# Performance work log

Measured on AMD Instinct MI355X. Metric: run time of the kernel, lower is better.

## Reference

```python
import jax, jax.numpy as jnp
import numpy as np
from jax import lax
import math

D_MODEL, D_STATE, D_CONV, D_INNER, DT_RANK = 1024, 16, 4, 2048, 64
BATCH, SEQLEN = 2, 2048


def setup_inputs() -> dict:
    key = jax.random.key(0)
    ks = jax.random.split(key, 10)
    s = 0.02
    x = jax.random.normal(ks[0], (BATCH, SEQLEN, D_MODEL), jnp.float32)
    W_in = jax.random.normal(ks[1], (D_MODEL, 2 * D_INNER), jnp.float32) * s
    conv_w = jax.random.normal(ks[2], (D_INNER, 1, D_CONV), jnp.float32) * 0.2
    conv_b = jnp.zeros((D_INNER,), jnp.float32)
    W_x = jax.random.normal(ks[3], (D_INNER, DT_RANK + 2 * D_STATE), jnp.float32) * s
    W_dt = jax.random.normal(ks[4], (DT_RANK, D_INNER), jnp.float32) * s
    # dt bias init as in the torch module: inverse-softplus of dt ~ logU(1e-3, 1e-1)
    u = jax.random.uniform(ks[5], (D_INNER,), jnp.float32)
    dt = jnp.clip(jnp.exp(u * (math.log(0.1) - math.log(0.001)) + math.log(0.001)), 1e-4)
    b_dt = dt + jnp.log(-jnp.expm1(-dt))
    A_log = jnp.log(jnp.tile(jnp.arange(1, D_STATE + 1, dtype=jnp.float32)[None, :], (D_INNER, 1)))
    D = jnp.ones((D_INNER,), jnp.float32)
    W_out = jax.random.normal(ks[6], (D_INNER, D_MODEL), jnp.float32) * s
    return {"x": x, "W_in": W_in, "conv_w": conv_w, "conv_b": conv_b, "W_x": W_x,
            "W_dt": W_dt, "b_dt": b_dt, "A_log": A_log, "D": D, "W_out": W_out}


def _forward(x, W_in, conv_w, conv_b, W_x, W_dt, b_dt, A_log, D, W_out):
    b, l, _ = x.shape
    d_inner, d_state = A_log.shape
    d_conv = conv_w.shape[-1]
    dt_rank = W_dt.shape[0]

    xz = x @ W_in                                  # (b, l, 2*d_inner)
    xi, z = jnp.split(xz, 2, axis=-1)

    # depthwise causal conv1d (torch pads both sides by d_conv-1 then slices [:l])
    xc = jnp.transpose(xi, (0, 2, 1))              # (b, d_inner, l)
    xc = lax.conv_general_dilated(
        xc, conv_w, window_strides=(1,), padding=[(d_conv - 1, 0)],
        feature_group_count=d_inner,
        dimension_numbers=("NCH", "OIH", "NCH"))
    xc = xc + conv_b[None, :, None]
    xi = jax.nn.silu(jnp.transpose(xc, (0, 2, 1)))  # (b, l, d_inner)

    x_dbl = xi @ W_x                                # (b, l, dt_rank + 2*d_state)
    dt, B, C = jnp.split(x_dbl, [dt_rank, dt_rank + d_state], axis=-1)
    dt = jax.nn.softplus(dt @ W_dt + b_dt)          # (b, l, d_inner)
    A = -jnp.exp(A_log)                             # (d_inner, d_state)

    def step(h, inp):
        dt_t, B_t, C_t, x_t = inp                   # (b,d),(b,n),(b,n),(b,d)
        dA = jnp.exp(dt_t[..., None] * A)           # (b, d, n)
        dB = dt_t[..., None] * B_t[:, None, :]      # (b, d, n)
        h = dA * h + dB * x_t[..., None]
        y = jnp.einsum("bdn,bn->bd", h, C_t) + D * x_t
        return h, y

    xs = (jnp.transpose(dt, (1, 0, 2)), jnp.transpose(B, (1, 0, 2)),
          jnp.transpose(C, (1, 0, 2)), jnp.transpose(xi, (1, 0, 2)))
    h0 = jnp.zeros((b, d_inner, d_state), x.dtype)
    _, ys = lax.scan(step, h0, xs)                  # ys: (l, b, d_inner)
    y = jnp.transpose(ys, (1, 0, 2))

    y = y * jax.nn.silu(z)
    return y @ W_out                                # (b, l, d_model)


def reference(x, W_in, conv_w, conv_b, W_x, W_dt, b_dt, A_log, D, W_out):
    return _forward(x, W_in, conv_w, conv_b, W_x, W_dt, b_dt, A_log, D, W_out)
```

## Files before the change

### kernel.cpp

```cpp
#include <hip/hip_runtime.h>
#include <math.h>


#define D_INNER 2048
#define D_STATE 16
#define SEQLEN  2048
#define NBATCH  2
#define NCHUNK  32
#define CHUNKLEN (SEQLEN / NCHUNK)

using f32x4 = __attribute__((ext_vector_type(4))) float;
using s16x8 = __attribute__((ext_vector_type(8))) short;

__device__ __forceinline__ float siluf(float x) {
  return x / (1.f + __expf(-x));
}
__device__ __forceinline__ float softplusf(float x) {
  return fmaxf(x, 0.f) + log1pf(__expf(-fabsf(x)));
}

__device__ __forceinline__ void split_pair(float f0, float f1,
                                           unsigned& hw, unsigned& lw) {
  unsigned b0 = __float_as_uint(f0), b1 = __float_as_uint(f1);
  hw = (b0 >> 16) | (b1 & 0xFFFF0000u);
  float r0 = f0 - __uint_as_float(b0 & 0xFFFF0000u);
  float r1 = f1 - __uint_as_float(b1 & 0xFFFF0000u);
  unsigned c0 = __float_as_uint(r0); c0 += 0x7FFFu + ((c0 >> 16) & 1u);
  unsigned c1 = __float_as_uint(r1); c1 += 0x7FFFu + ((c1 >> 16) & 1u);
  lw = (c0 >> 16) | (c1 & 0xFFFF0000u);
}

__global__ __launch_bounds__(256) void packsplit_k(
    const float* __restrict__ in, unsigned* __restrict__ out)
{
  size_t g = (size_t)blockIdx.x * 256 + threadIdx.x;
  float f[32];
#pragma unroll
  for (int q = 0; q < 8; ++q)
    *(float4*)&f[q * 4] = *(const float4*)(in + g * 32 + q * 4);
  unsigned* o = out + g * 32;
#pragma unroll
  for (int j = 0; j < 16; ++j) {
    unsigned hw, lw;
    split_pair(f[2 * j], f[2 * j + 1], hw, lw);
    o[j] = hw; o[16 + j] = lw;
  }
}

__global__ __launch_bounds__(256) void transpack_k(
    const float* __restrict__ in, unsigned* __restrict__ out, int K, int N)
{
  __shared__ float tile[32][257];
  const int tid = threadIdx.x;
  const int nb = blockIdx.x * 256;
  const int kc = blockIdx.y;
#pragma unroll 8
  for (int ky = 0; ky < 32; ++ky)
    tile[ky][tid] = in[(size_t)(kc * 32 + ky) * N + nb + tid];
  __syncthreads();
  unsigned* o = out + ((size_t)(nb + tid) * (K >> 5) + kc) * 32;
#pragma unroll
  for (int j = 0; j < 16; ++j) {
    unsigned hw, lw;
    split_pair(tile[2 * j][tid], tile[2 * j + 1][tid], hw, lw);
    o[j] = hw; o[16 + j] = lw;
  }
}

__global__ __launch_bounds__(128) void transpack_wx_k(
    const float* __restrict__ Wx, unsigned* __restrict__ out)
{
  const int n = threadIdx.x;
  const int kc = blockIdx.x;
  float f[32];
#pragma unroll
  for (int j = 0; j < 32; ++j)
    f[j] = (n < 96) ? Wx[(size_t)(kc * 32 + j) * 96 + n] : 0.f;
  unsigned* o = out + ((size_t)n * 64 + kc) * 32;
#pragma unroll
  for (int j = 0; j < 16; ++j) {
    unsigned hw, lw;
    split_pair(f[2 * j], f[2 * j + 1], hw, lw);
    o[j] = hw; o[16 + j] = lw;
  }
}

__global__ __launch_bounds__(256, 2) void mgemm_split(
    const unsigned short* __restrict__ A, const unsigned short* __restrict__ Bt,
    float* __restrict__ C, int M, int N, int K, int ldc)
{
  __shared__ s16x8 AsV[128 * 8];
  __shared__ s16x8 BsV[128 * 8];

  const int tid = threadIdx.x;
  const int wv  = tid >> 6;
  const int ln  = tid & 63;
  const int wr  = wv >> 1, wc = wv & 1;
  const int m0  = blockIdx.y * 128, n0 = blockIdx.x * 128;
  const int K32 = K >> 5;

  const int rr = ln & 15;
  const int ko = ln >> 4;
  const int sh = ko ^ (rr & 7);
  const int sl = (4 | ko) ^ (rr & 7);

  const int srow  = ln >> 3;
  const int sslot = (ln & 7) ^ srow;

  f32x4 acc[4][4];
#pragma unroll
  for (int i = 0; i < 4; i++)
#pragma unroll
    for (int j = 0; j < 4; j++) acc[i][j] = (f32x4)0.f;

  for (int ktc = 0; ktc < K32; ++ktc) {
    __syncthreads();
#pragma unroll
    for (int t = 0; t < 4; ++t) {
      int i = wv * 4 + t;
      const unsigned short* ga =
          A + ((size_t)(m0 + i * 8 + srow) * K32 + ktc) * 64 + sslot * 8;
      const unsigned short* gb =
          Bt + ((size_t)(n0 + i * 8 + srow) * K32 + ktc) * 64 + sslot * 8;
      __builtin_amdgcn_global_load_lds(
          (const __attribute__((address_space(1))) void*)ga,
          (__attribute__((address_space(3))) void*)((char*)AsV + i * 1024), 16, 0, 0);
      __builtin_amdgcn_global_load_lds(
          (const __attribute__((address_space(1))) void*)gb,
          (__attribute__((address_space(3))) void*)((char*)BsV + i * 1024), 16, 0, 0);
    }
    __syncthreads();

    s16x8 ah[4], al[4], bh[4], bl[4];
#pragma unroll
    for (int mi = 0; mi < 4; ++mi) {
      int r = wr * 64 + mi * 16 + rr;
      ah[mi] = AsV[r * 8 + sh];
      al[mi] = AsV[r * 8 + sl];
    }
#pragma unroll
    for (int ni = 0; ni < 4; ++ni) {
      int c = wc * 64 + ni * 16 + rr;
      bh[ni] = BsV[c * 8 + sh];
      bl[ni] = BsV[c * 8 + sl];
    }
#pragma unroll
    for (int mi = 0; mi < 4; ++mi)
#pragma unroll
      for (int ni = 0; ni < 4; ++ni) {
        acc[mi][ni] = __builtin_amdgcn_mfma_f32_16x16x32_bf16(ah[mi], bh[ni], acc[mi][ni], 0, 0, 0);
        acc[mi][ni] = __builtin_amdgcn_mfma_f32_16x16x32_bf16(ah[mi], bl[ni], acc[mi][ni], 0, 0, 0);
        acc[mi][ni] = __builtin_amdgcn_mfma_f32_16x16x32_bf16(al[mi], bh[ni], acc[mi][ni], 0, 0, 0);
      }
  }

  const int orow = (ln >> 4) * 4;
#pragma unroll
  for (int mi = 0; mi < 4; ++mi)
#pragma unroll
    for (int ni = 0; ni < 4; ++ni) {
      int rowg = m0 + wr * 64 + mi * 16 + orow;
      int colg = n0 + wc * 64 + ni * 16 + rr;
#pragma unroll
      for (int i = 0; i < 4; ++i)
        C[(size_t)(rowg + i) * ldc + colg] = acc[mi][ni][i];
    }
}

__global__ __launch_bounds__(256, 2) void xdbl_mfma_k(
    const unsigned short* __restrict__ A, const unsigned short* __restrict__ Bt,
    float* __restrict__ P)
{
  __shared__ s16x8 AsV[128 * 8];
  __shared__ s16x8 BsV[128 * 8];

  const int tid = threadIdx.x;
  const int wv  = tid >> 6;
  const int ln  = tid & 63;
  const int wr  = wv >> 1, wc = wv & 1;
  const int kz  = blockIdx.x;
  const int m0  = blockIdx.y * 128;
  const int K32 = 64;

  const int rr = ln & 15;
  const int ko = ln >> 4;
  const int sh = ko ^ (rr & 7);
  const int sl = (4 | ko) ^ (rr & 7);
  const int srow  = ln >> 3;
  const int sslot = (ln & 7) ^ srow;

  f32x4 acc[4][4];
#pragma unroll
  for (int i = 0; i < 4; i++)
#pragma unroll
    for (int j = 0; j < 4; j++) acc[i][j] = (f32x4)0.f;

  for (int ktc = kz * 8; ktc < kz * 8 + 8; ++ktc) {
    __syncthreads();
#pragma unroll
    for (int t = 0; t < 4; ++t) {
      int i = wv * 4 + t;
      const unsigned short* ga =
          A + ((size_t)(m0 + i * 8 + srow) * K32 + ktc) * 64 + sslot * 8;
      const unsigned short* gb =
          Bt + ((size_t)(i * 8 + srow) * K32 + ktc) * 64 + sslot * 8;
      __builtin_amdgcn_global_load_lds(
          (const __attribute__((address_space(1))) void*)ga,
          (__attribute__((address_space(3))) void*)((char*)AsV + i * 1024), 16, 0, 0);
      __builtin_amdgcn_global_load_lds(
          (const __attribute__((address_space(1))) void*)gb,
          (__attribute__((address_space(3))) void*)((char*)BsV + i * 1024), 16, 0, 0);
    }
    __syncthreads();

    s16x8 ah[4], al[4], bh[4], bl[4];
#pragma unroll
    for (int mi = 0; mi < 4; ++mi) {
      int r = wr * 64 + mi * 16 + rr;
      ah[mi] = AsV[r * 8 + sh];
      al[mi] = AsV[r * 8 + sl];
    }
#pragma unroll
    for (int ni = 0; ni < 4; ++ni) {
      int c = wc * 64 + ni * 16 + rr;
      bh[ni] = BsV[c * 8 + sh];
      bl[ni] = BsV[c * 8 + sl];
    }
#pragma unroll
    for (int mi = 0; mi < 4; ++mi)
#pragma unroll
      for (int ni = 0; ni < 4; ++ni) {
        acc[mi][ni] = __builtin_amdgcn_mfma_f32_16x16x32_bf16(ah[mi], bh[ni], acc[mi][ni], 0, 0, 0);
        acc[mi][ni] = __builtin_amdgcn_mfma_f32_16x16x32_bf16(ah[mi], bl[ni], acc[mi][ni], 0, 0, 0);
        acc[mi][ni] = __builtin_amdgcn_mfma_f32_16x16x32_bf16(al[mi], bh[ni], acc[mi][ni], 0, 0, 0);
      }
  }

  const int orow = (ln >> 4) * 4;
#pragma unroll
  for (int mi = 0; mi < 4; ++mi)
#pragma unroll
    for (int ni = 0; ni < 4; ++ni) {
      int rowg = m0 + wr * 64 + mi * 16 + orow;
      int colg = wc * 64 + ni * 16 + rr;
      if (colg < 96) {
#pragma unroll
        for (int i = 0; i < 4; ++i)
          P[((size_t)kz * 4096 + rowg + i) * 96 + colg] = acc[mi][ni][i];
      }
    }
}

__global__ __launch_bounds__(256) void xdbl_reduce_k(
    const float* __restrict__ P, float* __restrict__ xdbl)
{
  int i = blockIdx.x * 256 + threadIdx.x;
  float s = 0.f;
#pragma unroll
  for (int kz = 0; kz < 8; ++kz) s += P[(size_t)kz * 393216 + i];
  xdbl[i] = s;
}

template <int EPI>
__global__ __launch_bounds__(256, 2) void sgemm_k(
    const float* __restrict__ A, const float* __restrict__ B,
    const float* __restrict__ bias, float* __restrict__ C,
    int M, int N, int K, int lda, int ldb, int ldc)
{
  __shared__ float As[16][132];
  __shared__ float Bs[16][128];

  const int tid = threadIdx.x;
  const int m0 = blockIdx.y * 128;
  const int n0 = blockIdx.x * 128;
  const int tx = tid & 15;
  const int ty = tid >> 4;

  float acc[2][2][4][4];
#pragma unroll
  for (int a = 0; a < 2; a++)
#pragma unroll
    for (int b2 = 0; b2 < 2; b2++)
#pragma unroll
      for (int i = 0; i < 4; i++)
#pragma unroll
        for (int j = 0; j < 4; j++) acc[a][b2][i][j] = 0.f;

  for (int k0 = 0; k0 < K; k0 += 16) {
#pragma unroll
    for (int t = 0; t < 2; ++t) {
      int i = tid + t * 256;
      int row = i >> 2;
      int kq = (i & 3) * 4;
      float4 v = *(const float4*)(A + (size_t)(m0 + row) * lda + k0 + kq);
      As[kq + 0][row] = v.x; As[kq + 1][row] = v.y;
      As[kq + 2][row] = v.z; As[kq + 3][row] = v.w;
    }
#pragma unroll
    for (int t = 0; t < 2; ++t) {
      int i = tid + t * 256;
      int kr = i >> 5;
      int cq = (i & 31) * 4;
      *(float4*)&Bs[kr][cq] = *(const float4*)(B + (size_t)(k0 + kr) * ldb + n0 + cq);
    }
    __syncthreads();
#pragma unroll
    for (int kk = 0; kk < 16; ++kk) {
      float4 a0 = *(const float4*)&As[kk][ty * 4];
      float4 a1 = *(const float4*)&As[kk][64 + ty * 4];
      float4 b0 = *(const float4*)&Bs[kk][tx * 4];
      float4 b1 = *(const float4*)&Bs[kk][64 + tx * 4];
      float av[2][4] = {{a0.x, a0.y, a0.z, a0.w}, {a1.x, a1.y, a1.z, a1.w}};
      float bv[2][4] = {{b0.x, b0.y, b0.z, b0.w}, {b1.x, b1.y, b1.z, b1.w}};
#pragma unroll
      for (int a = 0; a < 2; a++)
#pragma unroll
        for (int i = 0; i < 4; i++)
#pragma unroll
          for (int b2 = 0; b2 < 2; b2++)
#pragma unroll
            for (int j = 0; j < 4; j++)
              acc[a][b2][i][j] = fmaf(av[a][i], bv[b2][j], acc[a][b2][i][j]);
    }
    __syncthreads();
  }

#pragma unroll
  for (int a = 0; a < 2; a++) {
#pragma unroll
    for (int i = 0; i < 4; i++) {
      int row = m0 + a * 64 + ty * 4 + i;
#pragma unroll
      for (int b2 = 0; b2 < 2; b2++) {
        int col = n0 + b2 * 64 + tx * 4;
        float4 v = make_float4(acc[a][b2][i][0], acc[a][b2][i][1],
                               acc[a][b2][i][2], acc[a][b2][i][3]);
        if (EPI == 1) {
          v.x = softplusf(v.x + bias[col + 0]);
          v.y = softplusf(v.y + bias[col + 1]);
          v.z = softplusf(v.z + bias[col + 2]);
          v.w = softplusf(v.w + bias[col + 3]);
        }
        *(float4*)(C + (size_t)row * ldc + col) = v;
      }
    }
  }
}

__global__ __launch_bounds__(256) void conv_silu_k(
    const float* __restrict__ xz, const float* __restrict__ cw,
    const float* __restrict__ cb, float* __restrict__ xi)
{
  int idx = blockIdx.x * 256 + threadIdx.x;
  int d = idx & (D_INNER - 1);
  int row = idx >> 11;
  int l = row & (SEQLEN - 1);
  float4 w = *(const float4*)(cw + d * 4);
  const float wv[4] = {w.x, w.y, w.z, w.w};
  float acc = cb[d];
#pragma unroll
  for (int j = 0; j < 4; j++) {
    int ll = l - 3 + j;
    if (ll >= 0)
      acc = fmaf(wv[j], xz[(size_t)(row - 3 + j) * 4096 + d], acc);
  }
  xi[idx] = siluf(acc);
}

__global__ __launch_bounds__(256) void aprep_k(const float* __restrict__ A_log,
                                               float* __restrict__ A2)
{
  int i = blockIdx.x * 256 + threadIdx.x;
  A2[i] = -__expf(A_log[i]);
}

__global__ __launch_bounds__(256) void scan_pass1(
    const float* __restrict__ dt, const float* __restrict__ xi,
    const float* __restrict__ xdbl, const float* __restrict__ A2,
    float* __restrict__ cP, float* __restrict__ cH)
{
  int d = blockIdx.x * 256 + threadIdx.x;
  int c = blockIdx.y;
  int b = blockIdx.z;
  float a2[D_STATE], h[D_STATE], P[D_STATE];
#pragma unroll
  for (int n = 0; n < D_STATE; n++) {
    a2[n] = A2[d * D_STATE + n];
    h[n] = 0.f;
    P[n] = 1.f;
  }
  int rowbase = b * SEQLEN + c * CHUNKLEN;
  for (int l = 0; l < CHUNKLEN; l++) {
    int row = rowbase + l;
    float dtv = dt[(size_t)row * D_INNER + d];
    float xv = xi[(size_t)row * D_INNER + d];
    float dtx = dtv * xv;
    const float* Bp = xdbl + (size_t)row * 96 + 64;
#pragma unroll
    for (int n = 0; n < D_STATE; n++) {
      float dA = __expf(dtv * a2[n]);
      P[n] *= dA;
      h[n] = fmaf(dA, h[n], dtx * Bp[n]);
    }
  }
  size_t base = ((size_t)(b * D_INNER + d) * NCHUNK + c) * D_STATE;
#pragma unroll
  for (int n = 0; n < D_STATE; n++) {
    cP[base + n] = P[n];
    cH[base + n] = h[n];
  }
}

__global__ __launch_bounds__(256) void scan_pass2(
    const float* __restrict__ cP, float* __restrict__ cH)
{
  int t = blockIdx.x * 256 + threadIdx.x;
  size_t base = (size_t)(t >> 4) * (NCHUNK * D_STATE) + (t & 15);
  float h = 0.f;
  for (int c = 0; c < NCHUNK; c++) {
    size_t idx = base + (size_t)c * D_STATE;
    float Pv = cP[idx];
    float q = cH[idx];
    cH[idx] = h;
    h = fmaf(Pv, h, q);
  }
}

__global__ __launch_bounds__(256) void scan_pass3(
    float* __restrict__ dtyg, const float* __restrict__ xi,
    const float* __restrict__ xdbl, const float* __restrict__ A2,
    const float* __restrict__ cH, const float* __restrict__ Dvec,
    const float* __restrict__ xz)
{
  int d = blockIdx.x * 256 + threadIdx.x;
  int c = blockIdx.y;
  int b = blockIdx.z;
  float a2[D_STATE], h[D_STATE];
  size_t base = ((size_t)(b * D_INNER + d) * NCHUNK + c) * D_STATE;
#pragma unroll
  for (int n = 0; n < D_STATE; n++) {
    a2[n] = A2[d * D_STATE + n];
    h[n] = cH[base + n];
  }
  float Dd = Dvec[d];
  int rowbase = b * SEQLEN + c * CHUNKLEN;
  for (int l = 0; l < CHUNKLEN; l++) {
    int row = rowbase + l;
    float dtv = dtyg[(size_t)row * D_INNER + d];
    float xv = xi[(size_t)row * D_INNER + d];
    float dtx = dtv * xv;
    const float* Bp = xdbl + (size_t)row * 96 + 64;
    const float* Cp = Bp + D_STATE;
    float y = Dd * xv;
#pragma unroll
    for (int n = 0; n < D_STATE; n++) {
      float dA = __expf(dtv * a2[n]);
      h[n] = fmaf(dA, h[n], dtx * Bp[n]);
      y = fmaf(h[n], Cp[n], y);
    }
    float z = xz[(size_t)row * 4096 + D_INNER + d];
    dtyg[(size_t)row * D_INNER + d] = y * siluf(z);
  }
}

extern "C" void kernel_launch(void* const* d_in, const int* in_sizes, int n_in,
                              void* d_out, int out_size, void* d_ws,
                              size_t ws_size, hipStream_t stream)
{
  const float* x     = (const float*)d_in[0];
  const float* W_in  = (const float*)d_in[1];
  const float* cw    = (const float*)d_in[2];
  const float* cb    = (const float*)d_in[3];
  const float* W_x   = (const float*)d_in[4];
  const float* W_dt  = (const float*)d_in[5];
  const float* b_dt  = (const float*)d_in[6];
  const float* A_log = (const float*)d_in[7];
  const float* Dv    = (const float*)d_in[8];
  const float* W_out = (const float*)d_in[9];
  float* out = (float*)d_out;

  float* ws    = (float*)d_ws;
  float* xz    = ws;
  float* xi    = xz + 16777216;
  float* xdbl  = xi + 8388608;
  float* dtyg  = xdbl + 393216;
  float* A2    = dtyg + 8388608;
  float* cP    = A2 + 32768;
  float* cH    = cP + 2097152;

  unsigned* WinTP  = (unsigned*)dtyg;
  unsigned* xP     = (unsigned*)(dtyg + 4194304);
  unsigned* xiP    = (unsigned*)dtyg;
  unsigned* WxTP   = (unsigned*)xdbl;
  float*    Ppart  = cP;
  unsigned* ygP    = (unsigned*)xi;
  unsigned* WoutTP = (unsigned*)cP;

  aprep_k<<<128, 256, 0, stream>>>(A_log, A2);

  transpack_k<<<dim3(16, 32), 256, 0, stream>>>(W_in, WinTP, 1024, 4096);
  packsplit_k<<<512, 256, 0, stream>>>(x, xP);

  mgemm_split<<<dim3(32, 32), 256, 0, stream>>>(
      (const unsigned short*)xP, (const unsigned short*)WinTP, xz,
      4096, 4096, 1024, 4096);

  conv_silu_k<<<32768, 256, 0, stream>>>(xz, cw, cb, xi);

  packsplit_k<<<1024, 256, 0, stream>>>(xi, xiP);
  transpack_wx_k<<<64, 128, 0, stream>>>(W_x, WxTP);
  xdbl_mfma_k<<<dim3(8, 32), 256, 0, stream>>>(
      (const unsigned short*)xiP, (const unsigned short*)WxTP, Ppart);
  xdbl_reduce_k<<<1536, 256, 0, stream>>>(Ppart, xdbl);

  sgemm_k<1><<<dim3(16, 32), 256, 0, stream>>>(xdbl, W_dt, b_dt, dtyg,
                                               4096, 2048, 64, 96, 2048, 2048);

  scan_pass1<<<dim3(8, NCHUNK, NBATCH), 256, 0, stream>>>(dtyg, xi, xdbl, A2, cP, cH);
  scan_pass2<<<256, 256, 0, stream>>>(cP, cH);
  scan_pass3<<<dim3(8, NCHUNK, NBATCH), 256, 0, stream>>>(dtyg, xi, xdbl, A2, cH, Dv, xz);

  packsplit_k<<<1024, 256, 0, stream>>>(dtyg, ygP);
  transpack_k<<<dim3(4, 64), 256, 0, stream>>>(W_out, WoutTP, 2048, 1024);

  mgemm_split<<<dim3(8, 32), 256, 0, stream>>>(
      (const unsigned short*)ygP, (const unsigned short*)WoutTP, out,
      4096, 1024, 2048, 1024);
}
```

Before: 478.8 us.

## Double-buffer LDS in split-bf16 MFMA GEMMs and fuse conv+SiLU with packing

Both split-bf16 MFMA GEMM kernels now use two LDS buffers and prefetch the next K-slice with global_load_lds while computing on the current one. This replaces the two barriers per iteration with a single wait and barrier at the end of each step. Separately, the depthwise conv+SiLU kernel is fused with the bf16 hi/lo packing of xi, removing one full read of xi and one kernel launch. Doubling LDS per block may lower occupancy, and the wait still drains all loads each iteration, so overlap is limited.

```diff
diff --git a/kernel.cpp b/kernel.cpp
--- a/kernel.cpp
+++ b/kernel.cpp
@@ -89,8 +89,8 @@
     const unsigned short* __restrict__ A, const unsigned short* __restrict__ Bt,
     float* __restrict__ C, int M, int N, int K, int ldc)
 {
-  __shared__ s16x8 AsV[128 * 8];
-  __shared__ s16x8 BsV[128 * 8];
+  __shared__ s16x8 AsV[2][128 * 8];
+  __shared__ s16x8 BsV[2][128 * 8];
 
   const int tid = threadIdx.x;
   const int wv  = tid >> 6;
@@ -103,18 +103,10 @@
   const int ko = ln >> 4;
   const int sh = ko ^ (rr & 7);
   const int sl = (4 | ko) ^ (rr & 7);
-
   const int srow  = ln >> 3;
   const int sslot = (ln & 7) ^ srow;
 
-  f32x4 acc[4][4];
-#pragma unroll
-  for (int i = 0; i < 4; i++)
-#pragma unroll
-    for (int j = 0; j < 4; j++) acc[i][j] = (f32x4)0.f;
-
-  for (int ktc = 0; ktc < K32; ++ktc) {
-    __syncthreads();
+  auto stage = [&](int buf, int ktc) {
 #pragma unroll
     for (int t = 0; t < 4; ++t) {
       int i = wv * 4 + t;
@@ -124,25 +116,39 @@
           Bt + ((size_t)(n0 + i * 8 + srow) * K32 + ktc) * 64 + sslot * 8;
       __builtin_amdgcn_global_load_lds(
           (const __attribute__((address_space(1))) void*)ga,
-          (__attribute__((address_space(3))) void*)((char*)AsV + i * 1024), 16, 0, 0);
+          (__attribute__((address_space(3))) void*)((char*)&AsV[buf][0] + i * 1024), 16, 0, 0);
       __builtin_amdgcn_global_load_lds(
           (const __attribute__((address_space(1))) void*)gb,
-          (__attribute__((address_space(3))) void*)((char*)BsV + i * 1024), 16, 0, 0);
-    }
-    __syncthreads();
+          (__attribute__((address_space(3))) void*)((char*)&BsV[buf][0] + i * 1024), 16, 0, 0);
+    }
+  };
+
+  f32x4 acc[4][4];
+#pragma unroll
+  for (int i = 0; i < 4; i++)
+#pragma unroll
+    for (int j = 0; j < 4; j++) acc[i][j] = (f32x4)0.f;
+
+  stage(0, 0);
+  asm volatile("s_waitcnt vmcnt(0)" ::: "memory");
+  __builtin_amdgcn_s_barrier();
+
+  int cur = 0;
+  for (int ktc = 0; ktc < K32; ++ktc) {
+    if (ktc + 1 < K32) stage(cur ^ 1, ktc + 1);
 
     s16x8 ah[4], al[4], bh[4], bl[4];
 #pragma unroll
     for (int mi = 0; mi < 4; ++mi) {
       int r = wr * 64 + mi * 16 + rr;
-      ah[mi] = AsV[r * 8 + sh];
-      al[mi] = AsV[r * 8 + sl];
+      ah[mi] = AsV[cur][r * 8 + sh];
+      al[mi] = AsV[cur][r * 8 + sl];
     }
 #pragma unroll
     for (int ni = 0; ni < 4; ++ni) {
       int c = wc * 64 + ni * 16 + rr;
-      bh[ni] = BsV[c * 8 + sh];
-      bl[ni] = BsV[c * 8 + sl];
+      bh[ni] = BsV[cur][c * 8 + sh];
+      bl[ni] = BsV[cur][c * 8 + sl];
     }
 #pragma unroll
     for (int mi = 0; mi < 4; ++mi)
@@ -152,6 +158,10 @@
         acc[mi][ni] = __builtin_amdgcn_mfma_f32_16x16x32_bf16(ah[mi], bl[ni], acc[mi][ni], 0, 0, 0);
         acc[mi][ni] = __builtin_amdgcn_mfma_f32_16x16x32_bf16(al[mi], bh[ni], acc[mi][ni], 0, 0, 0);
       }
+
+    asm volatile("s_waitcnt lgkmcnt(0) vmcnt(0)" ::: "memory");
+    __builtin_amdgcn_s_barrier();
+    cur ^= 1;
   }
 
   const int orow = (ln >> 4) * 4;
@@ -171,8 +181,8 @@
     const unsigned short* __restrict__ A, const unsigned short* __restrict__ Bt,
     float* __restrict__ P)
 {
-  __shared__ s16x8 AsV[128 * 8];
-  __shared__ s16x8 BsV[128 * 8];
+  __shared__ s16x8 AsV[2][128 * 8];
+  __shared__ s16x8 BsV[2][128 * 8];
 
   const int tid = threadIdx.x;
   const int wv  = tid >> 6;
@@ -189,14 +199,7 @@
   const int srow  = ln >> 3;
   const int sslot = (ln & 7) ^ srow;
 
-  f32x4 acc[4][4];
-#pragma unroll
-  for (int i = 0; i < 4; i++)
-#pragma unroll
-    for (int j = 0; j < 4; j++) acc[i][j] = (f32x4)0.f;
-
-  for (int ktc = kz * 8; ktc < kz * 8 + 8; ++ktc) {
-    __syncthreads();
+  auto stage = [&](int buf, int ktc) {
 #pragma unroll
     for (int t = 0; t < 4; ++t) {
       int i = wv * 4 + t;
@@ -206,25 +209,40 @@
           Bt + ((size_t)(i * 8 + srow) * K32 + ktc) * 64 + sslot * 8;
       __builtin_amdgcn_global_load_lds(
           (const __attribute__((address_space(1))) void*)ga,
-          (__attribute__((address_space(3))) void*)((char*)AsV + i * 1024), 16, 0, 0);
+          (__attribute__((address_space(3))) void*)((char*)&AsV[buf][0] + i * 1024), 16, 0, 0);
       __builtin_amdgcn_global_load_lds(
           (const __attribute__((address_space(1))) void*)gb,
-          (__attribute__((address_space(3))) void*)((char*)BsV + i * 1024), 16, 0, 0);
-    }
-    __syncthreads();
+          (__attribute__((address_space(3))) void*)((char*)&BsV[buf][0] + i * 1024), 16, 0, 0);
+    }
+  };
+
+  f32x4 acc[4][4];
+#pragma unroll
+  for (int i = 0; i < 4; i++)
+#pragma unroll
+    for (int j = 0; j < 4; j++) acc[i][j] = (f32x4)0.f;
+
+  const int kbeg = kz * 8, kend = kz * 8 + 8;
+  stage(0, kbeg);
+  asm volatile("s_waitcnt vmcnt(0)" ::: "memory");
+  __builtin_amdgcn_s_barrier();
+
+  int cur = 0;
+  for (int ktc = kbeg; ktc < kend; ++ktc) {
+    if (ktc + 1 < kend) stage(cur ^ 1, ktc + 1);
 
     s16x8 ah[4], al[4], bh[4], bl[4];
 #pragma unroll
     for (int mi = 0; mi < 4; ++mi) {
       int r = wr * 64 + mi * 16 + rr;
-      ah[mi] = AsV[r * 8 + sh];
-      al[mi] = AsV[r * 8 + sl];
+      ah[mi] = AsV[cur][r * 8 + sh];
+      al[mi] = AsV[cur][r * 8 + sl];
     }
 #pragma unroll
     for (int ni = 0; ni < 4; ++ni) {
       int c = wc * 64 + ni * 16 + rr;
-      bh[ni] = BsV[c * 8 + sh];
-      bl[ni] = BsV[c * 8 + sl];
+      bh[ni] = BsV[cur][c * 8 + sh];
+      bl[ni] = BsV[cur][c * 8 + sl];
     }
 #pragma unroll
     for (int mi = 0; mi < 4; ++mi)
@@ -234,6 +252,10 @@
         acc[mi][ni] = __builtin_amdgcn_mfma_f32_16x16x32_bf16(ah[mi], bl[ni], acc[mi][ni], 0, 0, 0);
         acc[mi][ni] = __builtin_amdgcn_mfma_f32_16x16x32_bf16(al[mi], bh[ni], acc[mi][ni], 0, 0, 0);
       }
+
+    asm volatile("s_waitcnt lgkmcnt(0) vmcnt(0)" ::: "memory");
+    __builtin_amdgcn_s_barrier();
+    cur ^= 1;
   }
 
   const int orow = (ln >> 4) * 4;
@@ -347,24 +369,58 @@
   }
 }
 
-__global__ __launch_bounds__(256) void conv_silu_k(
+__global__ __launch_bounds__(256) void conv_silu_pack_k(
     const float* __restrict__ xz, const float* __restrict__ cw,
-    const float* __restrict__ cb, float* __restrict__ xi)
-{
-  int idx = blockIdx.x * 256 + threadIdx.x;
-  int d = idx & (D_INNER - 1);
-  int row = idx >> 11;
+    const float* __restrict__ cb, float* __restrict__ xi,
+    unsigned* __restrict__ xiP)
+{
+  int g = blockIdx.x * 256 + threadIdx.x;
+  int ck = g & 63;
+  int row = g >> 6;
   int l = row & (SEQLEN - 1);
-  float4 w = *(const float4*)(cw + d * 4);
-  const float wv[4] = {w.x, w.y, w.z, w.w};
-  float acc = cb[d];
-#pragma unroll
-  for (int j = 0; j < 4; j++) {
-    int ll = l - 3 + j;
-    if (ll >= 0)
-      acc = fmaf(wv[j], xz[(size_t)(row - 3 + j) * 4096 + d], acc);
-  }
-  xi[idx] = siluf(acc);
+  int d0 = ck * 32;
+
+  float* xo = xi + (size_t)row * D_INNER + d0;
+  unsigned* po = xiP + (size_t)g * 32;
+
+#pragma unroll
+  for (int q = 0; q < 4; ++q) {
+    int dq = d0 + q * 8;
+    float acc[8];
+    float4 wv4[8];
+#pragma unroll
+    for (int e = 0; e < 8; ++e) {
+      wv4[e] = *(const float4*)(cw + (size_t)(dq + e) * 4);
+      acc[e] = cb[dq + e];
+    }
+#pragma unroll
+    for (int j = 0; j < 4; ++j) {
+      int ll = l - 3 + j;
+      if (ll >= 0) {
+        const float* src = xz + (size_t)(row - 3 + j) * 4096 + dq;
+        float4 v0 = *(const float4*)(src);
+        float4 v1 = *(const float4*)(src + 4);
+        float in[8] = {v0.x, v0.y, v0.z, v0.w, v1.x, v1.y, v1.z, v1.w};
+#pragma unroll
+        for (int e = 0; e < 8; ++e) {
+          float w = (j == 0) ? wv4[e].x : (j == 1) ? wv4[e].y
+                   : (j == 2) ? wv4[e].z : wv4[e].w;
+          acc[e] = fmaf(w, in[e], acc[e]);
+        }
+      }
+    }
+#pragma unroll
+    for (int e = 0; e < 8; ++e) acc[e] = siluf(acc[e]);
+    *(float4*)(xo + q * 8)     = make_float4(acc[0], acc[1], acc[2], acc[3]);
+    *(float4*)(xo + q * 8 + 4) = make_float4(acc[4], acc[5], acc[6], acc[7]);
+#pragma unroll
+    for (int p = 0; p < 4; ++p) {
+      unsigned hw, lw;
+      split_pair(acc[2 * p], acc[2 * p + 1], hw, lw);
+      po[q * 4 + p] = hw;
+      po[16 + q * 4 + p] = lw;
+    }
+  }
 }
 
 __global__ __launch_bounds__(256) void aprep_k(const float* __restrict__ A_log,
@@ -505,9 +561,8 @@
       (const unsigned short*)xP, (const unsigned short*)WinTP, xz,
       4096, 4096, 1024, 4096);
 
-  conv_silu_k<<<32768, 256, 0, stream>>>(xz, cw, cb, xi);
-
-  packsplit_k<<<1024, 256, 0, stream>>>(xi, xiP);
+  conv_silu_pack_k<<<1024, 256, 0, stream>>>(xz, cw, cb, xi, xiP);
+
   transpack_wx_k<<<64, 128, 0, stream>>>(W_x, WxTP);
   xdbl_mfma_k<<<dim3(8, 32), 256, 0, stream>>>(
       (const unsigned short*)xiP, (const unsigned short*)WxTP, Ppart);
```

New measurement: 535.6 us. +11.9%, slower.

## Double-buffer LDS tiles in split-bf16 GEMM kernels to overlap loads with MFMA

Applied to the files above, without the earlier changes.

Both the main split-bf16 GEMM and the x_dbl GEMM now keep two LDS buffers and prefetch the k-tile two steps ahead with global_load_lds. Partial vmcnt waits plus raw s_barrier replace the two __syncthreads per iteration. The aim is to hide global-memory latency behind the MFMA work. In exchange LDS use per block doubles, which may limit occupancy. Correctness also depends on the hand-chosen vmcnt count and on the ordering of LDS reads relative to the barriers.

```diff
diff --git a/kernel.cpp b/kernel.cpp
--- a/kernel.cpp
+++ b/kernel.cpp
@@ -89,8 +89,8 @@
     const unsigned short* __restrict__ A, const unsigned short* __restrict__ Bt,
     float* __restrict__ C, int M, int N, int K, int ldc)
 {
-  __shared__ s16x8 AsV[128 * 8];
-  __shared__ s16x8 BsV[128 * 8];
+  __shared__ s16x8 AsV[2][128 * 8];
+  __shared__ s16x8 BsV[2][128 * 8];
 
   const int tid = threadIdx.x;
   const int wv  = tid >> 6;
@@ -103,18 +103,10 @@
   const int ko = ln >> 4;
   const int sh = ko ^ (rr & 7);
   const int sl = (4 | ko) ^ (rr & 7);
-
   const int srow  = ln >> 3;
   const int sslot = (ln & 7) ^ srow;
 
-  f32x4 acc[4][4];
-#pragma unroll
-  for (int i = 0; i < 4; i++)
-#pragma unroll
-    for (int j = 0; j < 4; j++) acc[i][j] = (f32x4)0.f;
-
-  for (int ktc = 0; ktc < K32; ++ktc) {
-    __syncthreads();
+  auto stage = [&](int buf, int ktc) {
 #pragma unroll
     for (int t = 0; t < 4; ++t) {
       int i = wv * 4 + t;
@@ -124,25 +116,42 @@
           Bt + ((size_t)(n0 + i * 8 + srow) * K32 + ktc) * 64 + sslot * 8;
       __builtin_amdgcn_global_load_lds(
           (const __attribute__((address_space(1))) void*)ga,
-          (__attribute__((address_space(3))) void*)((char*)AsV + i * 1024), 16, 0, 0);
+          (__attribute__((address_space(3))) void*)((char*)&AsV[buf][0] + i * 1024), 16, 0, 0);
       __builtin_amdgcn_global_load_lds(
           (const __attribute__((address_space(1))) void*)gb,
-          (__attribute__((address_space(3))) void*)((char*)BsV + i * 1024), 16, 0, 0);
-    }
-    __syncthreads();
+          (__attribute__((address_space(3))) void*)((char*)&BsV[buf][0] + i * 1024), 16, 0, 0);
+    }
+  };
+
+  f32x4 acc[4][4];
+#pragma unroll
+  for (int i = 0; i < 4; i++)
+#pragma unroll
+    for (int j = 0; j < 4; j++) acc[i][j] = (f32x4)0.f;
+
+  stage(0, 0);
+  stage(1, 1);
+
+  int cur = 0;
+  for (int ktc = 0; ktc < K32; ++ktc) {
+    if (ktc + 1 < K32)
+      asm volatile("s_waitcnt vmcnt(8)" ::: "memory");
+    else
+      asm volatile("s_waitcnt vmcnt(0)" ::: "memory");
+    __builtin_amdgcn_s_barrier();
 
     s16x8 ah[4], al[4], bh[4], bl[4];
 #pragma unroll
     for (int mi = 0; mi < 4; ++mi) {
       int r = wr * 64 + mi * 16 + rr;
-      ah[mi] = AsV[r * 8 + sh];
-      al[mi] = AsV[r * 8 + sl];
+      ah[mi] = AsV[cur][r * 8 + sh];
+      al[mi] = AsV[cur][r * 8 + sl];
     }
 #pragma unroll
     for (int ni = 0; ni < 4; ++ni) {
       int c = wc * 64 + ni * 16 + rr;
-      bh[ni] = BsV[c * 8 + sh];
-      bl[ni] = BsV[c * 8 + sl];
+      bh[ni] = BsV[cur][c * 8 + sh];
+      bl[ni] = BsV[cur][c * 8 + sl];
     }
 #pragma unroll
     for (int mi = 0; mi < 4; ++mi)
@@ -152,6 +161,10 @@
         acc[mi][ni] = __builtin_amdgcn_mfma_f32_16x16x32_bf16(ah[mi], bl[ni], acc[mi][ni], 0, 0, 0);
         acc[mi][ni] = __builtin_amdgcn_mfma_f32_16x16x32_bf16(al[mi], bh[ni], acc[mi][ni], 0, 0, 0);
       }
+
+    __builtin_amdgcn_s_barrier();
+    if (ktc + 2 < K32) stage(cur, ktc + 2);
+    cur ^= 1;
   }
 
   const int orow = (ln >> 4) * 4;
@@ -171,8 +184,8 @@
     const unsigned short* __restrict__ A, const unsigned short* __restrict__ Bt,
     float* __restrict__ P)
 {
-  __shared__ s16x8 AsV[128 * 8];
-  __shared__ s16x8 BsV[128 * 8];
+  __shared__ s16x8 AsV[2][128 * 8];
+  __shared__ s16x8 BsV[2][128 * 8];
 
   const int tid = threadIdx.x;
   const int wv  = tid >> 6;
@@ -189,14 +202,7 @@
   const int srow  = ln >> 3;
   const int sslot = (ln & 7) ^ srow;
 
-  f32x4 acc[4][4];
-#pragma unroll
-  for (int i = 0; i < 4; i++)
-#pragma unroll
-    for (int j = 0; j < 4; j++) acc[i][j] = (f32x4)0.f;
-
-  for (int ktc = kz * 8; ktc < kz * 8 + 8; ++ktc) {
-    __syncthreads();
+  auto stage = [&](int buf, int ktc) {
 #pragma unroll
     for (int t = 0; t < 4; ++t) {
       int i = wv * 4 + t;
@@ -206,25 +212,43 @@
           Bt + ((size_t)(i * 8 + srow) * K32 + ktc) * 64 + sslot * 8;
       __builtin_amdgcn_global_load_lds(
           (const __attribute__((address_space(1))) void*)ga,
-          (__attribute__((address_space(3))) void*)((char*)AsV + i * 1024), 16, 0, 0);
+          (__attribute__((address_space(3))) void*)((char*)&AsV[buf][0] + i * 1024), 16, 0, 0);
       __builtin_amdgcn_global_load_lds(
           (const __attribute__((address_space(1))) void*)gb,
-          (__attribute__((address_space(3))) void*)((char*)BsV + i * 1024), 16, 0, 0);
-    }
-    __syncthreads();
+          (__attribute__((address_space(3))) void*)((char*)&BsV[buf][0] + i * 1024), 16, 0, 0);
+    }
+  };
+
+  f32x4 acc[4][4];
+#pragma unroll
+  for (int i = 0; i < 4; i++)
+#pragma unroll
+    for (int j = 0; j < 4; j++) acc[i][j] = (f32x4)0.f;
+
+  const int kbeg = kz * 8, kend = kz * 8 + 8;
+  stage(0, kbeg);
+  stage(1, kbeg + 1);
+
+  int cur = 0;
+  for (int ktc = kbeg; ktc < kend; ++ktc) {
+    if (ktc + 1 < kend)
+      asm volatile("s_waitcnt vmcnt(8)" ::: "memory");
+    else
+      asm volatile("s_waitcnt vmcnt(0)" ::: "memory");
+    __builtin_amdgcn_s_barrier();
 
     s16x8 ah[4], al[4], bh[4], bl[4];
 #pragma unroll
     for (int mi = 0; mi < 4; ++mi) {
       int r = wr * 64 + mi * 16 + rr;
-      ah[mi] = AsV[r * 8 + sh];
-      al[mi] = AsV[r * 8 + sl];
+      ah[mi] = AsV[cur][r * 8 + sh];
+      al[mi] = AsV[cur][r * 8 + sl];
     }
 #pragma unroll
     for (int ni = 0; ni < 4; ++ni) {
       int c = wc * 64 + ni * 16 + rr;
-      bh[ni] = BsV[c * 8 + sh];
-      bl[ni] = BsV[c * 8 + sl];
+      bh[ni] = BsV[cur][c * 8 + sh];
+      bl[ni] = BsV[cur][c * 8 + sl];
     }
 #pragma unroll
     for (int mi = 0; mi < 4; ++mi)
@@ -234,6 +258,10 @@
         acc[mi][ni] = __builtin_amdgcn_mfma_f32_16x16x32_bf16(ah[mi], bl[ni], acc[mi][ni], 0, 0, 0);
         acc[mi][ni] = __builtin_amdgcn_mfma_f32_16x16x32_bf16(al[mi], bh[ni], acc[mi][ni], 0, 0, 0);
       }
+
+    __builtin_amdgcn_s_barrier();
+    if (ktc + 2 < kend) stage(cur, ktc + 2);
+    cur ^= 1;
   }
 
   const int orow = (ln >> 4) * 4;
```

Measured after the change: 511.5 us. +6.8%, slower.
